# Kernel tuning notes

Hardware: AMD Instinct MI355X
Metric: run time of the kernel (lower is better)

Reference implementation:

```python
import jax, jax.numpy as jnp
import numpy as np

FP8_MAX = 448.0  # max representable magnitude of float8_e4m3fn
SCALE_EPS = 1e-7


def setup_inputs() -> dict:
    key = jax.random.key(0)
    k1, k2, k3 = jax.random.split(key, 3)
    in_f, out_f = 2048, 2048
    x = jax.random.normal(k1, (4, 4096, in_f), dtype=jnp.float32)
    # weight is stored in fp8 in the torch module; materialize fp8-representable fp32 values
    w_fp32 = jax.random.normal(k2, (out_f, in_f), dtype=jnp.float32) * (1.0 / np.sqrt(in_f))
    weight = w_fp32.astype(jnp.float8_e4m3fn).astype(jnp.float32)
    weight_scale = jnp.ones((), dtype=jnp.float32)
    bound = 1.0 / np.sqrt(in_f)
    bias = jax.random.uniform(k3, (out_f,), dtype=jnp.float32, minval=-bound, maxval=bound)
    return {"x": x, "weight": weight, "weight_scale": weight_scale, "bias": bias}


def reference(x, weight, weight_scale, bias):
    # per-tensor dynamic fp8 quantization of the input (scale = absmax / 448)
    scale = jnp.maximum(jnp.max(jnp.abs(x)) / FP8_MAX, SCALE_EPS)
    x_q = (x / scale).astype(jnp.float8_e4m3fn).astype(jnp.float32)
    # dequantize weight (fp8 values stored as fp32 here) with its per-tensor scale
    w = weight * weight_scale
    # NOTE: faithful to the source, the output is NOT rescaled by the input scale
    # (the original forward drops input_scale after quantization).
    out = jnp.einsum('bsi,oi->bso', x_q, w) + bias
    return out
```

## Files before the change

### kernel.cpp

```cpp
#include <hip/hip_runtime.h>
#include <hip/hip_bf16.h>

typedef __attribute__((ext_vector_type(4))) float floatx4;
typedef __attribute__((ext_vector_type(8))) int   intx8;

#define FP8_MAX_F 448.0f
#define SCALE_EPS 1e-7f

__global__ void k_absmax(const float* __restrict__ x, unsigned* __restrict__ amax, int n4) {
    __shared__ float wmax[4];
    int tid = blockIdx.x * blockDim.x + threadIdx.x;
    int stride = gridDim.x * blockDim.x;
    const float4* x4 = (const float4*)x;
    float m = 0.f;
    for (int i = tid; i < n4; i += stride) {
        float4 v = x4[i];
        m = fmaxf(fmaxf(fabsf(v.x), fabsf(v.y)),
                  fmaxf(m, fmaxf(fabsf(v.z), fabsf(v.w))));
    }
    #pragma unroll
    for (int off = 32; off > 0; off >>= 1) m = fmaxf(m, __shfl_xor(m, off, 64));
    if ((threadIdx.x & 63) == 0) wmax[threadIdx.x >> 6] = m;
    __syncthreads();
    if (threadIdx.x == 0) {
        float t = fmaxf(fmaxf(wmax[0], wmax[1]), fmaxf(wmax[2], wmax[3]));
        atomicMax(amax, __float_as_uint(t));
    }
}

__global__ void k_quant_w(const float* __restrict__ w, int* __restrict__ wq, int n16) {
    int tid = blockIdx.x * blockDim.x + threadIdx.x;
    int stride = gridDim.x * blockDim.x;
    const float4* x4 = (const float4*)w;
    int4* q4 = (int4*)wq;
    for (int i = tid; i < n16; i += stride) {
        float4 v0 = x4[4*i], v1 = x4[4*i+1], v2 = x4[4*i+2], v3 = x4[4*i+3];
        int4 o;
        o.x = __builtin_amdgcn_cvt_pk_fp8_f32(v0.x, v0.y, 0, false);
        o.x = __builtin_amdgcn_cvt_pk_fp8_f32(v0.z, v0.w, o.x, true);
        o.y = __builtin_amdgcn_cvt_pk_fp8_f32(v1.x, v1.y, 0, false);
        o.y = __builtin_amdgcn_cvt_pk_fp8_f32(v1.z, v1.w, o.y, true);
        o.z = __builtin_amdgcn_cvt_pk_fp8_f32(v2.x, v2.y, 0, false);
        o.z = __builtin_amdgcn_cvt_pk_fp8_f32(v2.z, v2.w, o.z, true);
        o.w = __builtin_amdgcn_cvt_pk_fp8_f32(v3.x, v3.y, 0, false);
        o.w = __builtin_amdgcn_cvt_pk_fp8_f32(v3.z, v3.w, o.w, true);
        q4[i] = o;
    }
}

__global__ void k_quant_x(const float* __restrict__ x, int* __restrict__ xq,
                          const unsigned* __restrict__ amax, int n16) {
    float scale = fmaxf(__uint_as_float(*amax) / FP8_MAX_F, SCALE_EPS);
    int tid = blockIdx.x * blockDim.x + threadIdx.x;
    int stride = gridDim.x * blockDim.x;
    const float4* x4 = (const float4*)x;
    int4* q4 = (int4*)xq;
    for (int i = tid; i < n16; i += stride) {
        float4 v0 = x4[4*i], v1 = x4[4*i+1], v2 = x4[4*i+2], v3 = x4[4*i+3];
        int4 o;
        o.x = __builtin_amdgcn_cvt_pk_fp8_f32(v0.x / scale, v0.y / scale, 0, false);
        o.x = __builtin_amdgcn_cvt_pk_fp8_f32(v0.z / scale, v0.w / scale, o.x, true);
        o.y = __builtin_amdgcn_cvt_pk_fp8_f32(v1.x / scale, v1.y / scale, 0, false);
        o.y = __builtin_amdgcn_cvt_pk_fp8_f32(v1.z / scale, v1.w / scale, o.y, true);
        o.z = __builtin_amdgcn_cvt_pk_fp8_f32(v2.x / scale, v2.y / scale, 0, false);
        o.z = __builtin_amdgcn_cvt_pk_fp8_f32(v2.z / scale, v2.w / scale, o.z, true);
        o.w = __builtin_amdgcn_cvt_pk_fp8_f32(v3.x / scale, v3.y / scale, 0, false);
        o.w = __builtin_amdgcn_cvt_pk_fp8_f32(v3.z / scale, v3.w / scale, o.w, true);
        q4[i] = o;
    }
}

#define BM 256
#define BN 256
#define BKQ 128
#define NT 16

#define GLOAD(src, dst) \
    __builtin_amdgcn_global_load_lds((const __attribute__((address_space(1))) void*)(src), \
                                     (__attribute__((address_space(3))) void*)(dst), 16, 0, 0)
#define BARRIER()  asm volatile("s_barrier" ::: "memory")
#define WAIT_VM(n) asm volatile("s_waitcnt vmcnt(" #n ")" ::: "memory")
#define WAIT_LGKM() asm volatile("s_waitcnt lgkmcnt(0)" ::: "memory")

#define LDFRAG(dstv, pL, pH, IMM) {                      \
    int4 lo_ = *(const int4*)((pL) + (IMM));             \
    int4 hi_ = *(const int4*)((pH) + (IMM));             \
    dstv = (intx8){lo_.x, lo_.y, lo_.z, lo_.w, hi_.x, hi_.y, hi_.z, hi_.w}; }

#define MFMA_ROW(m, af)                                                            \
    acc[m][0] = __builtin_amdgcn_mfma_scale_f32_16x16x128_f8f6f4(                  \
        af, b[0], acc[m][0], 0, 0, 0, 0x7F7F7F7F, 0, 0x7F7F7F7F);                  \
    acc[m][1] = __builtin_amdgcn_mfma_scale_f32_16x16x128_f8f6f4(                  \
        af, b[1], acc[m][1], 0, 0, 0, 0x7F7F7F7F, 0, 0x7F7F7F7F);                  \
    acc[m][2] = __builtin_amdgcn_mfma_scale_f32_16x16x128_f8f6f4(                  \
        af, b[2], acc[m][2], 0, 0, 0, 0x7F7F7F7F, 0, 0x7F7F7F7F);                  \
    acc[m][3] = __builtin_amdgcn_mfma_scale_f32_16x16x128_f8f6f4(                  \
        af, b[3], acc[m][3], 0, 0, 0, 0x7F7F7F7F, 0, 0x7F7F7F7F);

__global__ __launch_bounds__(512, 2) void k_gemm_mx(
    const unsigned char* __restrict__ A, const unsigned char* __restrict__ B,
    const float* __restrict__ bias, const float* __restrict__ wscale,
    float* __restrict__ C, int M, int N, int K) {
    __shared__ __align__(16) unsigned char lds[131072];

    int nwg = gridDim.x;
    int bid = blockIdx.x;
    bid = (bid & 7) * (nwg >> 3) + (bid >> 3);
    int ntn = N / BN;
    int tm = bid / ntn, tn = bid % ntn;
    int row0 = tm * BM, col0 = tn * BN;

    int tid = (int)threadIdx.x;
    int lane = tid & 63, wid = tid >> 6;
    int wr = wid >> 2, wc = wid & 3;
    int fr = lane & 15, g = lane >> 4;

    int srow = tid >> 3;
    int sc   = (tid & 7) ^ (srow & 7);
    const int offA0 = (row0 + srow) * K + sc * 16;
    const int offB0 = (col0 + srow) * K + sc * 16;
    unsigned char* dstA = lds + tid * 16;
    unsigned char* dstB = dstA + 32768;

    int c0 = (2 * g) ^ (fr & 7);
    const int aL = wr * 16384 + fr * 128 + c0 * 16;
    const int aH = wr * 16384 + fr * 128 + (c0 ^ 1) * 16;
    const int bL = 32768 + wc * 8192 + fr * 128 + c0 * 16;
    const int bH = 32768 + wc * 8192 + fr * 128 + (c0 ^ 1) * 16;

    floatx4 acc[8][4];
    #pragma unroll
    for (int m = 0; m < 8; ++m)
        #pragma unroll
        for (int n = 0; n < 4; ++n) acc[m][n] = (floatx4)(0.f);

    GLOAD(A + offA0,          dstA);
    GLOAD(A + offA0 + 131072, dstA + 8192);
    GLOAD(A + offA0 + 262144, dstA + 16384);
    GLOAD(A + offA0 + 393216, dstA + 24576);
    GLOAD(B + offB0,          dstB);
    GLOAD(B + offB0 + 131072, dstB + 8192);
    GLOAD(B + offB0 + 262144, dstB + 16384);
    GLOAD(B + offB0 + 393216, dstB + 24576);

    for (int t = 0; t < NT; ++t) {
        const int bufo = (t & 1) << 16;
        const int nbufo = bufo ^ 65536;
        const unsigned char* AbL = lds + bufo + aL;
        const unsigned char* AbH = lds + bufo + aH;
        const unsigned char* BbL = lds + bufo + bL;
        const unsigned char* BbH = lds + bufo + bH;
        unsigned char* dA = dstA + nbufo;
        unsigned char* dB = dstB + nbufo;
        const int kn = ((t + 1) & (NT - 1)) * BKQ;

        intx8 b[4], a0, a1;

        GLOAD(A + kn + offA0,          dA);
        GLOAD(A + kn + offA0 + 131072, dA + 8192);
        GLOAD(B + kn + offB0,          dB);
        GLOAD(B + kn + offB0 + 131072, dB + 8192);
        WAIT_VM(4);
        BARRIER();
        LDFRAG(b[0], BbL, BbH, 0)
        LDFRAG(b[1], BbL, BbH, 2048)
        LDFRAG(b[2], BbL, BbH, 4096)
        LDFRAG(b[3], BbL, BbH, 6144)
        LDFRAG(a0, AbL, AbH, 0)
        LDFRAG(a1, AbL, AbH, 2048)
        WAIT_LGKM();
        __builtin_amdgcn_sched_barrier(0);
        __builtin_amdgcn_s_setprio(1);
        MFMA_ROW(0, a0)
        MFMA_ROW(1, a1)
        __builtin_amdgcn_s_setprio(0);
        BARRIER();

        GLOAD(A + kn + offA0 + 262144, dA + 16384);
        GLOAD(A + kn + offA0 + 393216, dA + 24576);
        GLOAD(B + kn + offB0 + 262144, dB + 16384);
        GLOAD(B + kn + offB0 + 393216, dB + 24576);
        LDFRAG(a0, AbL, AbH, 4096)
        LDFRAG(a1, AbL, AbH, 6144)
        BARRIER();
        WAIT_LGKM();
        __builtin_amdgcn_sched_barrier(0);
        __builtin_amdgcn_s_setprio(1);
        MFMA_ROW(2, a0)
        MFMA_ROW(3, a1)
        __builtin_amdgcn_s_setprio(0);
        BARRIER();

        LDFRAG(a0, AbL, AbH, 8192)
        LDFRAG(a1, AbL, AbH, 10240)
        BARRIER();
        WAIT_LGKM();
        __builtin_amdgcn_sched_barrier(0);
        __builtin_amdgcn_s_setprio(1);
        MFMA_ROW(4, a0)
        MFMA_ROW(5, a1)
        __builtin_amdgcn_s_setprio(0);
        BARRIER();

        LDFRAG(a0, AbL, AbH, 12288)
        LDFRAG(a1, AbL, AbH, 14336)
        BARRIER();
        WAIT_LGKM();
        __builtin_amdgcn_sched_barrier(0);
        __builtin_amdgcn_s_setprio(1);
        MFMA_ROW(6, a0)
        MFMA_ROW(7, a1)
        __builtin_amdgcn_s_setprio(0);
        BARRIER();
    }

    WAIT_VM(0);

    float wsv = *wscale;
    int crow = (lane >> 4) * 4;
    int ccol = lane & 15;
    float bv[4];
    #pragma unroll
    for (int n = 0; n < 4; ++n) bv[n] = bias[col0 + wc * 64 + n * 16 + ccol];
    #pragma unroll
    for (int m = 0; m < 8; ++m) {
        int r = row0 + wr * 128 + m * 16 + crow;
        #pragma unroll
        for (int n = 0; n < 4; ++n) {
            int c = col0 + wc * 64 + n * 16 + ccol;
            #pragma unroll
            for (int j = 0; j < 4; ++j)
                C[(long)(r + j) * N + c] = acc[m][n][j] * wsv + bv[n];
        }
    }
}

extern "C" void kernel_launch(void* const* d_in, const int* in_sizes, int n_in,
                              void* d_out, int out_size, void* d_ws, size_t ws_size,
                              hipStream_t stream) {
    const float* x      = (const float*)d_in[0];
    const float* w      = (const float*)d_in[1];
    const float* wscale = (const float*)d_in[2];
    const float* bias   = (const float*)d_in[3];
    float* out = (float*)d_out;

    const int K = 2048, N = 2048;
    const int M = in_sizes[0] / K;

    unsigned char* ws = (unsigned char*)d_ws;
    unsigned* amax = (unsigned*)ws;
    int* wq = (int*)(ws + 1024);
    int* xq = (int*)(ws + 1024 + (size_t)N * K);

    hipMemsetAsync(amax, 0, 4, stream);
    k_absmax<<<2048, 256, 0, stream>>>(x, amax, (M * K) / 4);
    k_quant_w<<<1024, 256, 0, stream>>>(w, wq, (N * K) / 16);
    k_quant_x<<<2048, 256, 0, stream>>>(x, xq, amax, (M * K) / 16);

    int grid = (M / BM) * (N / BN);
    k_gemm_mx<<<grid, 512, 0, stream>>>((const unsigned char*)xq, (const unsigned char*)wq,
                                        bias, wscale, out, M, N, K);
}
```

Measured before the change: 177.9 us.

## Issue all tile loads upfront and double-buffer A fragments with partial LDS waits

```diff
diff --git a/kernel.cpp b/kernel.cpp
--- a/kernel.cpp
+++ b/kernel.cpp
@@ -78,9 +78,10 @@
 #define GLOAD(src, dst) \
     __builtin_amdgcn_global_load_lds((const __attribute__((address_space(1))) void*)(src), \
                                      (__attribute__((address_space(3))) void*)(dst), 16, 0, 0)
-#define BARRIER()  asm volatile("s_barrier" ::: "memory")
-#define WAIT_VM(n) asm volatile("s_waitcnt vmcnt(" #n ")" ::: "memory")
-#define WAIT_LGKM() asm volatile("s_waitcnt lgkmcnt(0)" ::: "memory")
+#define BARRIER()   asm volatile("s_barrier" ::: "memory")
+#define WAIT_VM(n)  asm volatile("s_waitcnt vmcnt(" #n ")" ::: "memory")
+#define WAIT_LGKM(n) asm volatile("s_waitcnt lgkmcnt(" #n ")" ::: "memory")
+#define SB0()       __builtin_amdgcn_sched_barrier(0)
 
 #define LDFRAG(dstv, pL, pH, IMM) {                      \
     int4 lo_ = *(const int4*)((pL) + (IMM));             \
@@ -89,13 +90,13 @@
 
 #define MFMA_ROW(m, af)                                                            \
     acc[m][0] = __builtin_amdgcn_mfma_scale_f32_16x16x128_f8f6f4(                  \
-        af, b[0], acc[m][0], 0, 0, 0, 0x7F7F7F7F, 0, 0x7F7F7F7F);                  \
+        af, b0, acc[m][0], 0, 0, 0, 0x7F7F7F7F, 0, 0x7F7F7F7F);                    \
     acc[m][1] = __builtin_amdgcn_mfma_scale_f32_16x16x128_f8f6f4(                  \
-        af, b[1], acc[m][1], 0, 0, 0, 0x7F7F7F7F, 0, 0x7F7F7F7F);                  \
+        af, b1, acc[m][1], 0, 0, 0, 0x7F7F7F7F, 0, 0x7F7F7F7F);                    \
     acc[m][2] = __builtin_amdgcn_mfma_scale_f32_16x16x128_f8f6f4(                  \
-        af, b[2], acc[m][2], 0, 0, 0, 0x7F7F7F7F, 0, 0x7F7F7F7F);                  \
+        af, b2, acc[m][2], 0, 0, 0, 0x7F7F7F7F, 0, 0x7F7F7F7F);                    \
     acc[m][3] = __builtin_amdgcn_mfma_scale_f32_16x16x128_f8f6f4(                  \
-        af, b[3], acc[m][3], 0, 0, 0, 0x7F7F7F7F, 0, 0x7F7F7F7F);
+        af, b3, acc[m][3], 0, 0, 0, 0x7F7F7F7F, 0, 0x7F7F7F7F);
 
 __global__ __launch_bounds__(512, 2) void k_gemm_mx(
     const unsigned char* __restrict__ A, const unsigned char* __restrict__ B,
@@ -143,6 +144,7 @@
     GLOAD(B + offB0 + 262144, dstB + 16384);
     GLOAD(B + offB0 + 393216, dstB + 24576);
 
+    #pragma unroll 2
     for (int t = 0; t < NT; ++t) {
         const int bufo = (t & 1) << 16;
         const int nbufo = bufo ^ 65536;
@@ -154,62 +156,51 @@
         unsigned char* dB = dstB + nbufo;
         const int kn = ((t + 1) & (NT - 1)) * BKQ;
 
-        intx8 b[4], a0, a1;
-
         GLOAD(A + kn + offA0,          dA);
         GLOAD(A + kn + offA0 + 131072, dA + 8192);
+        GLOAD(A + kn + offA0 + 262144, dA + 16384);
+        GLOAD(A + kn + offA0 + 393216, dA + 24576);
         GLOAD(B + kn + offB0,          dB);
         GLOAD(B + kn + offB0 + 131072, dB + 8192);
-        WAIT_VM(4);
-        BARRIER();
-        LDFRAG(b[0], BbL, BbH, 0)
-        LDFRAG(b[1], BbL, BbH, 2048)
-        LDFRAG(b[2], BbL, BbH, 4096)
-        LDFRAG(b[3], BbL, BbH, 6144)
-        LDFRAG(a0, AbL, AbH, 0)
-        LDFRAG(a1, AbL, AbH, 2048)
-        WAIT_LGKM();
-        __builtin_amdgcn_sched_barrier(0);
-        __builtin_amdgcn_s_setprio(1);
-        MFMA_ROW(0, a0)
-        MFMA_ROW(1, a1)
-        __builtin_amdgcn_s_setprio(0);
-        BARRIER();
-
-        GLOAD(A + kn + offA0 + 262144, dA + 16384);
-        GLOAD(A + kn + offA0 + 393216, dA + 24576);
         GLOAD(B + kn + offB0 + 262144, dB + 16384);
         GLOAD(B + kn + offB0 + 393216, dB + 24576);
-        LDFRAG(a0, AbL, AbH, 4096)
-        LDFRAG(a1, AbL, AbH, 6144)
+        SB0();
+        WAIT_VM(8);
+        SB0();
         BARRIER();
-        WAIT_LGKM();
-        __builtin_amdgcn_sched_barrier(0);
-        __builtin_amdgcn_s_setprio(1);
-        MFMA_ROW(2, a0)
-        MFMA_ROW(3, a1)
-        __builtin_amdgcn_s_setprio(0);
-        BARRIER();
-
-        LDFRAG(a0, AbL, AbH, 8192)
-        LDFRAG(a1, AbL, AbH, 10240)
-        BARRIER();
-        WAIT_LGKM();
-        __builtin_amdgcn_sched_barrier(0);
-        __builtin_amdgcn_s_setprio(1);
-        MFMA_ROW(4, a0)
-        MFMA_ROW(5, a1)
-        __builtin_amdgcn_s_setprio(0);
-        BARRIER();
-
-        LDFRAG(a0, AbL, AbH, 12288)
-        LDFRAG(a1, AbL, AbH, 14336)
-        BARRIER();
-        WAIT_LGKM();
-        __builtin_amdgcn_sched_barrier(0);
-        __builtin_amdgcn_s_setprio(1);
-        MFMA_ROW(6, a0)
-        MFMA_ROW(7, a1)
+
+        intx8 b0, b1, b2, b3, aP0, aP1, aQ0, aQ1;
+        LDFRAG(b0, BbL, BbH, 0)
+        LDFRAG(b1, BbL, BbH, 2048)
+        LDFRAG(b2, BbL, BbH, 4096)
+        LDFRAG(b3, BbL, BbH, 6144)
+        LDFRAG(aP0, AbL, AbH, 0)
+        LDFRAG(aP1, AbL, AbH, 2048)
+        LDFRAG(aQ0, AbL, AbH, 4096)
+        LDFRAG(aQ1, AbL, AbH, 6144)
+        SB0(); WAIT_LGKM(4); SB0();
+        __builtin_amdgcn_s_setprio(1);
+        MFMA_ROW(0, aP0)
+        MFMA_ROW(1, aP1)
+        __builtin_amdgcn_s_setprio(0);
+        LDFRAG(aP0, AbL, AbH, 8192)
+        LDFRAG(aP1, AbL, AbH, 10240)
+        SB0(); WAIT_LGKM(4); SB0();
+        __builtin_amdgcn_s_setprio(1);
+        MFMA_ROW(2, aQ0)
+        MFMA_ROW(3, aQ1)
+        __builtin_amdgcn_s_setprio(0);
+        LDFRAG(aQ0, AbL, AbH, 12288)
+        LDFRAG(aQ1, AbL, AbH, 14336)
+        SB0(); WAIT_LGKM(4); SB0();
+        __builtin_amdgcn_s_setprio(1);
+        MFMA_ROW(4, aP0)
+        MFMA_ROW(5, aP1)
+        __builtin_amdgcn_s_setprio(0);
+        SB0(); WAIT_LGKM(0); SB0();
+        __builtin_amdgcn_s_setprio(1);
+        MFMA_ROW(6, aQ0)
+        MFMA_ROW(7, aQ1)
         __builtin_amdgcn_s_setprio(0);
         BARRIER();
     }
```

Measured after the change: 164.0 us. 1.08x faster.

## Merge absmax and weight-quant kernels; spread GEMM prefetch loads across phases

Applied to the files above, without the earlier changes.

```diff
diff --git a/kernel.cpp b/kernel.cpp
--- a/kernel.cpp
+++ b/kernel.cpp
@@ -7,44 +7,45 @@
 #define FP8_MAX_F 448.0f
 #define SCALE_EPS 1e-7f
 
-__global__ void k_absmax(const float* __restrict__ x, unsigned* __restrict__ amax, int n4) {
-    __shared__ float wmax[4];
-    int tid = blockIdx.x * blockDim.x + threadIdx.x;
-    int stride = gridDim.x * blockDim.x;
-    const float4* x4 = (const float4*)x;
-    float m = 0.f;
-    for (int i = tid; i < n4; i += stride) {
-        float4 v = x4[i];
-        m = fmaxf(fmaxf(fabsf(v.x), fabsf(v.y)),
-                  fmaxf(m, fmaxf(fabsf(v.z), fabsf(v.w))));
-    }
-    #pragma unroll
-    for (int off = 32; off > 0; off >>= 1) m = fmaxf(m, __shfl_xor(m, off, 64));
-    if ((threadIdx.x & 63) == 0) wmax[threadIdx.x >> 6] = m;
-    __syncthreads();
-    if (threadIdx.x == 0) {
-        float t = fmaxf(fmaxf(wmax[0], wmax[1]), fmaxf(wmax[2], wmax[3]));
-        atomicMax(amax, __float_as_uint(t));
-    }
-}
-
-__global__ void k_quant_w(const float* __restrict__ w, int* __restrict__ wq, int n16) {
-    int tid = blockIdx.x * blockDim.x + threadIdx.x;
-    int stride = gridDim.x * blockDim.x;
-    const float4* x4 = (const float4*)w;
-    int4* q4 = (int4*)wq;
-    for (int i = tid; i < n16; i += stride) {
-        float4 v0 = x4[4*i], v1 = x4[4*i+1], v2 = x4[4*i+2], v3 = x4[4*i+3];
-        int4 o;
-        o.x = __builtin_amdgcn_cvt_pk_fp8_f32(v0.x, v0.y, 0, false);
-        o.x = __builtin_amdgcn_cvt_pk_fp8_f32(v0.z, v0.w, o.x, true);
-        o.y = __builtin_amdgcn_cvt_pk_fp8_f32(v1.x, v1.y, 0, false);
-        o.y = __builtin_amdgcn_cvt_pk_fp8_f32(v1.z, v1.w, o.y, true);
-        o.z = __builtin_amdgcn_cvt_pk_fp8_f32(v2.x, v2.y, 0, false);
-        o.z = __builtin_amdgcn_cvt_pk_fp8_f32(v2.z, v2.w, o.z, true);
-        o.w = __builtin_amdgcn_cvt_pk_fp8_f32(v3.x, v3.y, 0, false);
-        o.w = __builtin_amdgcn_cvt_pk_fp8_f32(v3.z, v3.w, o.w, true);
-        q4[i] = o;
+__global__ void k_pre(const float* __restrict__ x, unsigned* __restrict__ amax, int n4,
+                      const float* __restrict__ w, int* __restrict__ wq, int nw16) {
+    if (blockIdx.x < 1792) {
+        __shared__ float wmax[4];
+        int tid = blockIdx.x * 256 + threadIdx.x;
+        int stride = 1792 * 256;
+        const float4* x4 = (const float4*)x;
+        float m = 0.f;
+        for (int i = tid; i < n4; i += stride) {
+            float4 v = x4[i];
+            m = fmaxf(fmaxf(fabsf(v.x), fabsf(v.y)),
+                      fmaxf(m, fmaxf(fabsf(v.z), fabsf(v.w))));
+        }
+        #pragma unroll
+        for (int off = 32; off > 0; off >>= 1) m = fmaxf(m, __shfl_xor(m, off, 64));
+        if ((threadIdx.x & 63) == 0) wmax[threadIdx.x >> 6] = m;
+        __syncthreads();
+        if (threadIdx.x == 0) {
+            float t = fmaxf(fmaxf(wmax[0], wmax[1]), fmaxf(wmax[2], wmax[3]));
+            atomicMax(amax, __float_as_uint(t));
+        }
+    } else {
+        int tid = (blockIdx.x - 1792) * 256 + threadIdx.x;
+        int stride = 256 * 256;
+        const float4* x4 = (const float4*)w;
+        int4* q4 = (int4*)wq;
+        for (int i = tid; i < nw16; i += stride) {
+            float4 v0 = x4[4*i], v1 = x4[4*i+1], v2 = x4[4*i+2], v3 = x4[4*i+3];
+            int4 o;
+            o.x = __builtin_amdgcn_cvt_pk_fp8_f32(v0.x, v0.y, 0, false);
+            o.x = __builtin_amdgcn_cvt_pk_fp8_f32(v0.z, v0.w, o.x, true);
+            o.y = __builtin_amdgcn_cvt_pk_fp8_f32(v1.x, v1.y, 0, false);
+            o.y = __builtin_amdgcn_cvt_pk_fp8_f32(v1.z, v1.w, o.y, true);
+            o.z = __builtin_amdgcn_cvt_pk_fp8_f32(v2.x, v2.y, 0, false);
+            o.z = __builtin_amdgcn_cvt_pk_fp8_f32(v2.z, v2.w, o.z, true);
+            o.w = __builtin_amdgcn_cvt_pk_fp8_f32(v3.x, v3.y, 0, false);
+            o.w = __builtin_amdgcn_cvt_pk_fp8_f32(v3.z, v3.w, o.w, true);
+            q4[i] = o;
+        }
     }
 }
 
@@ -78,9 +79,9 @@
 #define GLOAD(src, dst) \
     __builtin_amdgcn_global_load_lds((const __attribute__((address_space(1))) void*)(src), \
                                      (__attribute__((address_space(3))) void*)(dst), 16, 0, 0)
-#define BARRIER()  asm volatile("s_barrier" ::: "memory")
-#define WAIT_VM(n) asm volatile("s_waitcnt vmcnt(" #n ")" ::: "memory")
-#define WAIT_LGKM() asm volatile("s_waitcnt lgkmcnt(0)" ::: "memory")
+#define BARRIER()    asm volatile("s_barrier" ::: "memory")
+#define WAIT_VM(n)   asm volatile("s_waitcnt vmcnt(" #n ")" ::: "memory")
+#define WAIT_LGKM()  asm volatile("s_waitcnt lgkmcnt(0)" ::: "memory")
 
 #define LDFRAG(dstv, pL, pH, IMM) {                      \
     int4 lo_ = *(const int4*)((pL) + (IMM));             \
@@ -89,13 +90,13 @@
 
 #define MFMA_ROW(m, af)                                                            \
     acc[m][0] = __builtin_amdgcn_mfma_scale_f32_16x16x128_f8f6f4(                  \
-        af, b[0], acc[m][0], 0, 0, 0, 0x7F7F7F7F, 0, 0x7F7F7F7F);                  \
+        af, b0, acc[m][0], 0, 0, 0, 0x7F7F7F7F, 0, 0x7F7F7F7F);                    \
     acc[m][1] = __builtin_amdgcn_mfma_scale_f32_16x16x128_f8f6f4(                  \
-        af, b[1], acc[m][1], 0, 0, 0, 0x7F7F7F7F, 0, 0x7F7F7F7F);                  \
+        af, b1, acc[m][1], 0, 0, 0, 0x7F7F7F7F, 0, 0x7F7F7F7F);                    \
     acc[m][2] = __builtin_amdgcn_mfma_scale_f32_16x16x128_f8f6f4(                  \
-        af, b[2], acc[m][2], 0, 0, 0, 0x7F7F7F7F, 0, 0x7F7F7F7F);                  \
+        af, b2, acc[m][2], 0, 0, 0, 0x7F7F7F7F, 0, 0x7F7F7F7F);                    \
     acc[m][3] = __builtin_amdgcn_mfma_scale_f32_16x16x128_f8f6f4(                  \
-        af, b[3], acc[m][3], 0, 0, 0, 0x7F7F7F7F, 0, 0x7F7F7F7F);
+        af, b3, acc[m][3], 0, 0, 0, 0x7F7F7F7F, 0, 0x7F7F7F7F);
 
 __global__ __launch_bounds__(512, 2) void k_gemm_mx(
     const unsigned char* __restrict__ A, const unsigned char* __restrict__ B,
@@ -154,59 +155,55 @@
         unsigned char* dB = dstB + nbufo;
         const int kn = ((t + 1) & (NT - 1)) * BKQ;
 
-        intx8 b[4], a0, a1;
+        intx8 b0, b1, b2, b3, a0, a1;
 
         GLOAD(A + kn + offA0,          dA);
         GLOAD(A + kn + offA0 + 131072, dA + 8192);
+        WAIT_VM(2);
+        BARRIER();
+        LDFRAG(b0, BbL, BbH, 0)
+        LDFRAG(b1, BbL, BbH, 2048)
+        LDFRAG(b2, BbL, BbH, 4096)
+        LDFRAG(b3, BbL, BbH, 6144)
+        LDFRAG(a0, AbL, AbH, 0)
+        LDFRAG(a1, AbL, AbH, 2048)
+        WAIT_LGKM();
+        __builtin_amdgcn_s_setprio(1);
+        MFMA_ROW(0, a0)
+        MFMA_ROW(1, a1)
+        __builtin_amdgcn_s_setprio(0);
+        BARRIER();
+
+        LDFRAG(a0, AbL, AbH, 4096)
+        LDFRAG(a1, AbL, AbH, 6144)
+        GLOAD(A + kn + offA0 + 262144, dA + 16384);
+        GLOAD(A + kn + offA0 + 393216, dA + 24576);
+        BARRIER();
+        WAIT_LGKM();
+        __builtin_amdgcn_s_setprio(1);
+        MFMA_ROW(2, a0)
+        MFMA_ROW(3, a1)
+        __builtin_amdgcn_s_setprio(0);
+        BARRIER();
+
+        LDFRAG(a0, AbL, AbH, 8192)
+        LDFRAG(a1, AbL, AbH, 10240)
         GLOAD(B + kn + offB0,          dB);
         GLOAD(B + kn + offB0 + 131072, dB + 8192);
-        WAIT_VM(4);
-        BARRIER();
-        LDFRAG(b[0], BbL, BbH, 0)
-        LDFRAG(b[1], BbL, BbH, 2048)
-        LDFRAG(b[2], BbL, BbH, 4096)
-        LDFRAG(b[3], BbL, BbH, 6144)
-        LDFRAG(a0, AbL, AbH, 0)
-        LDFRAG(a1, AbL, AbH, 2048)
-        WAIT_LGKM();
-        __builtin_amdgcn_sched_barrier(0);
-        __builtin_amdgcn_s_setprio(1);
-        MFMA_ROW(0, a0)
-        MFMA_ROW(1, a1)
-        __builtin_amdgcn_s_setprio(0);
-        BARRIER();
-
-        GLOAD(A + kn + offA0 + 262144, dA + 16384);
-        GLOAD(A + kn + offA0 + 393216, dA + 24576);
+        BARRIER();
+        WAIT_LGKM();
+        __builtin_amdgcn_s_setprio(1);
+        MFMA_ROW(4, a0)
+        MFMA_ROW(5, a1)
+        __builtin_amdgcn_s_setprio(0);
+        BARRIER();
+
+        LDFRAG(a0, AbL, AbH, 12288)
+        LDFRAG(a1, AbL, AbH, 14336)
         GLOAD(B + kn + offB0 + 262144, dB + 16384);
         GLOAD(B + kn + offB0 + 393216, dB + 24576);
-        LDFRAG(a0, AbL, AbH, 4096)
-        LDFRAG(a1, AbL, AbH, 6144)
-        BARRIER();
-        WAIT_LGKM();
-        __builtin_amdgcn_sched_barrier(0);
-        __builtin_amdgcn_s_setprio(1);
-        MFMA_ROW(2, a0)
-        MFMA_ROW(3, a1)
-        __builtin_amdgcn_s_setprio(0);
-        BARRIER();
-
-        LDFRAG(a0, AbL, AbH, 8192)
-        LDFRAG(a1, AbL, AbH, 10240)
-        BARRIER();
-        WAIT_LGKM();
-        __builtin_amdgcn_sched_barrier(0);
-        __builtin_amdgcn_s_setprio(1);
-        MFMA_ROW(4, a0)
-        MFMA_ROW(5, a1)
-        __builtin_amdgcn_s_setprio(0);
-        BARRIER();
-
-        LDFRAG(a0, AbL, AbH, 12288)
-        LDFRAG(a1, AbL, AbH, 14336)
-        BARRIER();
-        WAIT_LGKM();
-        __builtin_amdgcn_sched_barrier(0);
+        BARRIER();
+        WAIT_LGKM();
         __builtin_amdgcn_s_setprio(1);
         MFMA_ROW(6, a0)
         MFMA_ROW(7, a1)
@@ -253,8 +250,7 @@
     int* xq = (int*)(ws + 1024 + (size_t)N * K);
 
     hipMemsetAsync(amax, 0, 4, stream);
-    k_absmax<<<2048, 256, 0, stream>>>(x, amax, (M * K) / 4);
-    k_quant_w<<<1024, 256, 0, stream>>>(w, wq, (N * K) / 16);
+    k_pre<<<2048, 256, 0, stream>>>(x, amax, (M * K) / 4, w, wq, (N * K) / 16);
     k_quant_x<<<2048, 256, 0, stream>>>(x, xq, amax, (M * K) / 16);
 
     int grid = (M / BM) * (N / BN);
```

After: 154.3 us. 1.15x faster.
